# Kernel optimization log

Measured on AMD Instinct MI355X. Metric: run time of the kernel, lower is better.

## Reference

```python
import jax, jax.numpy as jnp
import numpy as np

N, F_IN, F_OUT = 8192, 512, 256
NEG_BIG = -9e15


def setup_inputs() -> dict:
    key = jax.random.key(0)
    k1, k2, k3, k4, k5 = jax.random.split(key, 5)
    h = jax.random.normal(k1, (N, F_IN), dtype=jnp.float32)
    adj = jax.random.randint(k2, (N, N), 0, 2, dtype=jnp.int32)
    W = jax.random.normal(k3, (F_IN, F_OUT), dtype=jnp.float32) / np.sqrt(F_IN)
    bW = jnp.zeros((F_OUT,), dtype=jnp.float32)
    a1 = jax.random.normal(k4, (F_OUT,), dtype=jnp.float32) / np.sqrt(2 * F_OUT)
    a2 = jax.random.normal(k5, (F_OUT,), dtype=jnp.float32) / np.sqrt(2 * F_OUT)
    ba = jnp.zeros((), dtype=jnp.float32)
    return {"h": h, "adj": adj, "W": W, "bW": bW, "a1": a1, "a2": a2, "ba": ba}


def reference(h, adj, W, bW, a1, a2, ba):
    # Wh: [N, F_OUT]
    Wh = h @ W + bW
    # a([Wh_i ; Wh_j]) + b == (Wh_i . a1) + (Wh_j . a2) + b  (rank-1 decomposition,
    # avoids the O(N^2 * 2F) repeat/cat tensor the torch code materializes)
    f1 = Wh @ a1  # [N]
    f2 = Wh @ a2  # [N]
    e = jax.nn.leaky_relu(f1[:, None] + f2[None, :] + ba, negative_slope=0.2)
    e = jnp.where(adj > 0, e, NEG_BIG)
    attention = jax.nn.softmax(e, axis=1)  # dropout = identity (eval mode)
    return attention @ Wh
```

## Files before the change

kernel.cpp:

```cpp
#include <hip/hip_runtime.h>

typedef __bf16 bf16;
typedef __attribute__((ext_vector_type(4))) float f32x4;
typedef __attribute__((ext_vector_type(8))) __bf16 bf16x8;
typedef __attribute__((ext_vector_type(4))) __bf16 bf16x4;
typedef __attribute__((ext_vector_type(4))) int i32x4;

#define NN 8192
#define FI 512
#define FO 256
#define NSPLIT 4
#define JCHUNK (NN / NSPLIT)

__global__ __launch_bounds__(256) void kw_split(const float* __restrict__ W,
                                                bf16* __restrict__ wth,
                                                bf16* __restrict__ wtl) {
  const int idx = blockIdx.x * 256 + threadIdx.x;
  const int k = idx >> 8, n = idx & 255;
  float x = W[idx];
  bf16 hi = (bf16)x;
  wth[(size_t)n * FI + k] = hi;
  wtl[(size_t)n * FI + k] = (bf16)(x - (float)hi);
}

__global__ __launch_bounds__(256, 2) void k1_gemm(
    const float* __restrict__ h, const bf16* __restrict__ wth,
    const bf16* __restrict__ wtl, const float* __restrict__ bW,
    const float* __restrict__ a1, const float* __restrict__ a2,
    bf16* __restrict__ whb, float* __restrict__ f1, float* __restrict__ f2) {
  __shared__ bf16 stg[128 * 32];
  const int t = threadIdx.x;
  const int lane = t & 63, w = t >> 6;
  const int m16 = lane & 15, q = lane >> 4;
  const int wr = w & 1, wn = w >> 1;
  const int rb = blockIdx.x, bj = blockIdx.y;
  const int row = rb * 32 + wr * 16 + m16;
  const int nb = bj * 128 + wn * 64;

  const f32x4 z4 = {0.f, 0.f, 0.f, 0.f};
  f32x4 acc[4];
#pragma unroll
  for (int nn = 0; nn < 4; ++nn) acc[nn] = z4;

  const float* hrow = h + (size_t)row * FI + q * 8;
  const bf16* wthp = wth + (size_t)(nb + m16) * FI + q * 8;
  const bf16* wtlp = wtl + (size_t)(nb + m16) * FI + q * 8;

  f32x4 nh0 = *(const f32x4*)(hrow);
  f32x4 nh1 = *(const f32x4*)(hrow + 4);

  const int KT = FI / 32;
  for (int kt = 0; kt < KT; ++kt) {
    bf16x8 bh[4], bl[4];
#pragma unroll
    for (int nn = 0; nn < 4; ++nn) {
      const size_t woff = (size_t)(nn * 16) * FI + kt * 32;
      bh[nn] = *(const bf16x8*)(wthp + woff);
      bl[nn] = *(const bf16x8*)(wtlp + woff);
    }
    const f32x4 h0 = nh0, h1 = nh1;
    const int ktn = (kt + 1 < KT) ? kt + 1 : kt;
    nh0 = *(const f32x4*)(hrow + ktn * 32);
    nh1 = *(const f32x4*)(hrow + ktn * 32 + 4);
    bf16x8 hh, hl;
#pragma unroll
    for (int x = 0; x < 4; ++x) {
      float v = h0[x];
      bf16 hi = (bf16)v;
      hh[x] = hi;
      hl[x] = (bf16)(v - (float)hi);
      float v2 = h1[x];
      bf16 hi2 = (bf16)v2;
      hh[4 + x] = hi2;
      hl[4 + x] = (bf16)(v2 - (float)hi2);
    }
#pragma unroll
    for (int nn = 0; nn < 4; ++nn) {
      acc[nn] = __builtin_amdgcn_mfma_f32_16x16x32_bf16(hh, bh[nn], acc[nn], 0, 0, 0);
      acc[nn] = __builtin_amdgcn_mfma_f32_16x16x32_bf16(hl, bh[nn], acc[nn], 0, 0, 0);
      acc[nn] = __builtin_amdgcn_mfma_f32_16x16x32_bf16(hh, bl[nn], acc[nn], 0, 0, 0);
    }
  }
  float f1p[4] = {}, f2p[4] = {};
  const int il = wr * 16 + q * 4;
#pragma unroll
  for (int nn = 0; nn < 4; ++nn) {
    const int n = nb + nn * 16 + m16;
    const int nl = wn * 64 + nn * 16 + m16;
    const float bw = bW[n], av1 = a1[n], av2 = a2[n];
    bf16x4 st;
#pragma unroll
    for (int reg = 0; reg < 4; ++reg) {
      float wh = acc[nn][reg] + bw;
      st[reg] = (bf16)wh;
      f1p[reg] += wh * av1;
      f2p[reg] += wh * av2;
    }
    *(bf16x4*)&stg[nl * 32 + il] = st;
  }
#pragma unroll
  for (int m = 1; m < 16; m <<= 1) {
#pragma unroll
    for (int reg = 0; reg < 4; ++reg) {
      f1p[reg] += __shfl_xor(f1p[reg], m);
      f2p[reg] += __shfl_xor(f2p[reg], m);
    }
  }
  if (m16 == 0) {
#pragma unroll
    for (int reg = 0; reg < 4; ++reg) {
      const int i = rb * 32 + wr * 16 + q * 4 + reg;
      atomicAdd(&f1[i], f1p[reg]);
      atomicAdd(&f2[i], f2p[reg]);
    }
  }
  __syncthreads();
  bf16x8* dst = (bf16x8*)(whb + (size_t)rb * (FO * 32) + (size_t)bj * (128 * 32));
  const bf16x8* srcv = (const bf16x8*)stg;
#pragma unroll
  for (int u = 0; u < 2; ++u) dst[t * 2 + u] = srcv[t * 2 + u];
}

__global__ __launch_bounds__(256, 4) void k4_attn(
    const int* __restrict__ adj, const bf16* __restrict__ whb,
    const float* __restrict__ f1, const float* __restrict__ f2,
    const float* __restrict__ ba_p,
    float* __restrict__ acc_part, float* __restrict__ l_part) {
  const int t = threadIdx.x;
  const int lane = t & 63, w = t >> 6;
  const int m16 = lane & 15, q = lane >> 4;
  const int wr = w & 1, wn = w >> 1;
  const int rb = blockIdx.x, s = blockIdx.y;
  const int i0 = rb * 32;
  const int row = i0 + wr * 16 + m16;

  const float ba = *ba_p;
  const float ci = f1[row] + ba;
  const float arg0 = ci + 8.0f;
  const float sh = fmaxf(arg0, 0.2f * arg0);

  const f32x4 z4 = {0.f, 0.f, 0.f, 0.f};
  f32x4 acc[8];
#pragma unroll
  for (int nn = 0; nn < 8; ++nn) acc[nn] = z4;
  float lreg = 0.f;

  const int sbase = s * JCHUNK;
  const int* arow = adj + (size_t)row * NN + sbase + q * 8;
  const float* frow = f2 + sbase + q * 8;
  const bf16* bptr = whb + (size_t)(sbase >> 5) * (FO * 32) +
                     (size_t)(wn * 128 + m16) * 32 + q * 8;

  i32x4 na0 = *(const i32x4*)(arow);
  i32x4 na1 = *(const i32x4*)(arow + 4);
  f32x4 nf0 = *(const f32x4*)(frow);
  f32x4 nf1 = *(const f32x4*)(frow + 4);

  const int KT = JCHUNK / 32;
  for (int kt = 0; kt < KT; ++kt) {
    bf16x8 cb[8];
    const bf16* bk = bptr + (size_t)kt * (FO * 32);
#pragma unroll
    for (int nn = 0; nn < 8; ++nn)
      cb[nn] = *(const bf16x8*)(bk + nn * (16 * 32));
    const i32x4 ca0 = na0;
    const i32x4 ca1 = na1;
    const f32x4 cf0 = nf0;
    const f32x4 cf1 = nf1;
    const int ktn = (kt + 1 < KT) ? kt + 1 : kt;
    na0 = *(const i32x4*)(arow + ktn * 32);
    na1 = *(const i32x4*)(arow + ktn * 32 + 4);
    nf0 = *(const f32x4*)(frow + ktn * 32);
    nf1 = *(const f32x4*)(frow + ktn * 32 + 4);
    float pv[8];
#pragma unroll
    for (int x = 0; x < 4; ++x) {
      float arg = ci + cf0[x];
      float e = fmaxf(arg, 0.2f * arg);
      pv[x] = (ca0[x] > 0) ? __expf(e - sh) : 0.f;
      float arg2 = ci + cf1[x];
      float e2 = fmaxf(arg2, 0.2f * arg2);
      pv[4 + x] = (ca1[x] > 0) ? __expf(e2 - sh) : 0.f;
    }
    bf16x8 af;
#pragma unroll
    for (int x = 0; x < 8; ++x) {
      lreg += pv[x];
      af[x] = (bf16)pv[x];
    }
#pragma unroll
    for (int nn = 0; nn < 8; ++nn)
      acc[nn] = __builtin_amdgcn_mfma_f32_16x16x32_bf16(af, cb[nn], acc[nn], 0, 0, 0);
  }
  lreg += __shfl_xor(lreg, 16);
  lreg += __shfl_xor(lreg, 32);
  if (q == 0 && wn == 0) l_part[(size_t)s * NN + row] = lreg;
  float* ap = acc_part + (size_t)s * ((size_t)NN * FO);
  const int r0 = i0 + wr * 16 + q * 4;
#pragma unroll
  for (int nn = 0; nn < 8; ++nn) {
    const int n = wn * 128 + nn * 16 + m16;
#pragma unroll
    for (int reg = 0; reg < 4; ++reg) {
      ap[(size_t)(r0 + reg) * FO + n] = acc[nn][reg];
    }
  }
}

__global__ __launch_bounds__(256) void k5_reduce(
    const float* __restrict__ accp, const float* __restrict__ lp,
    float* __restrict__ out) {
  const int idx = blockIdx.x * 256 + threadIdx.x;
  const int i = idx >> 6, n4 = (idx & 63) * 4;
  f32x4 sum = {0.f, 0.f, 0.f, 0.f};
  float l = 0.f;
#pragma unroll
  for (int s = 0; s < NSPLIT; ++s) {
    sum += *(const f32x4*)&accp[(size_t)s * ((size_t)NN * FO) + (size_t)i * FO + n4];
    l += lp[s * NN + i];
  }
  const float rl = 1.0f / l;
  f32x4 o = sum * rl;
  *(f32x4*)&out[(size_t)i * FO + n4] = o;
}

extern "C" void kernel_launch(void* const* d_in, const int* in_sizes, int n_in,
                              void* d_out, int out_size, void* d_ws, size_t ws_size,
                              hipStream_t stream) {
  const float* h   = (const float*)d_in[0];
  const int*   adj = (const int*)d_in[1];
  const float* W   = (const float*)d_in[2];
  const float* bW  = (const float*)d_in[3];
  const float* a1  = (const float*)d_in[4];
  const float* a2  = (const float*)d_in[5];
  const float* ba  = (const float*)d_in[6];
  float* out = (float*)d_out;

  char* ws = (char*)d_ws;
  bf16* whb   = (bf16*)ws;
  float* f1   = (float*)(ws + 4u * 1024 * 1024);
  float* f2   = (float*)(ws + 4u * 1024 * 1024 + 32 * 1024);
  float* accp = (float*)(ws + 4u * 1024 * 1024 + 64 * 1024);
  float* lp   = accp + (size_t)NSPLIT * NN * FO;
  bf16* wth   = (bf16*)((char*)lp + (size_t)NSPLIT * NN * 4);
  bf16* wtl   = wth + (size_t)FO * FI;

  hipMemsetAsync(f1, 0, 64 * 1024, stream);

  kw_split<<<FI * FO / 256, 256, 0, stream>>>(W, wth, wtl);
  k1_gemm<<<dim3(NN / 32, 2), 256, 0, stream>>>(h, wth, wtl, bW, a1, a2, whb, f1, f2);
  k4_attn<<<dim3(NN / 32, NSPLIT), 256, 0, stream>>>(adj, whb, f1, f2, ba, accp, lp);
  k5_reduce<<<(NN * FO / 4) / 256, 256, 0, stream>>>(accp, lp, out);
}
```

Measured before the change: 559.0 us.

## Split attention into score-materialization pass and full-K bf16 GEMM, drop split-K reduce

The fused attention kernel with a 4-way split-K and a separate reduce is replaced by two kernels. The first computes masked exp scores from adj and stores them as a bf16 P matrix in MFMA fragment layout, accumulating row sums atomically. The second runs a full-K GEMM of P against Wh, double-buffering its register loads, and writes normalized output directly. This removes the fp32 partial-accumulator writes and the reduce kernel, and gives the GEMM a cleaner load stream. The cost is a 128MB bf16 P write and re-read in exchange for the fp32 partials.

```diff
diff --git a/kernel.cpp b/kernel.cpp
--- a/kernel.cpp
+++ b/kernel.cpp
@@ -9,8 +9,8 @@
 #define NN 8192
 #define FI 512
 #define FO 256
-#define NSPLIT 4
-#define JCHUNK (NN / NSPLIT)
+
+#define MFMA16 __builtin_amdgcn_mfma_f32_16x16x32_bf16
 
 __global__ __launch_bounds__(256) void kw_split(const float* __restrict__ W,
                                                 bf16* __restrict__ wth,
@@ -76,9 +76,9 @@
     }
 #pragma unroll
     for (int nn = 0; nn < 4; ++nn) {
-      acc[nn] = __builtin_amdgcn_mfma_f32_16x16x32_bf16(hh, bh[nn], acc[nn], 0, 0, 0);
-      acc[nn] = __builtin_amdgcn_mfma_f32_16x16x32_bf16(hl, bh[nn], acc[nn], 0, 0, 0);
-      acc[nn] = __builtin_amdgcn_mfma_f32_16x16x32_bf16(hh, bl[nn], acc[nn], 0, 0, 0);
+      acc[nn] = MFMA16(hh, bh[nn], acc[nn], 0, 0, 0);
+      acc[nn] = MFMA16(hl, bh[nn], acc[nn], 0, 0, 0);
+      acc[nn] = MFMA16(hh, bl[nn], acc[nn], 0, 0, 0);
     }
   }
   float f1p[4] = {}, f2p[4] = {};
@@ -121,107 +121,125 @@
   for (int u = 0; u < 2; ++u) dst[t * 2 + u] = srcv[t * 2 + u];
 }
 
-__global__ __launch_bounds__(256, 4) void k4_attn(
-    const int* __restrict__ adj, const bf16* __restrict__ whb,
-    const float* __restrict__ f1, const float* __restrict__ f2,
-    const float* __restrict__ ba_p,
-    float* __restrict__ acc_part, float* __restrict__ l_part) {
+__global__ __launch_bounds__(256) void k4a_scores(
+    const int* __restrict__ adj, const float* __restrict__ f1,
+    const float* __restrict__ f2, const float* __restrict__ ba_p,
+    bf16* __restrict__ P, float* __restrict__ l) {
+  const int t = threadIdx.x;
+  const int lane = t & 63, w = t >> 6;
+  const int m16 = lane & 15, q = lane >> 4;
+  const int gw = blockIdx.x * 4 + w;
+  const int ib = gw >> 4;
+  const int js = gw & 15;
+  const int row = ib * 16 + m16;
+  const int j0 = js * 512;
+
+  const float ba = *ba_p;
+  const float ci = f1[row] + ba;
+  const float arg0 = ci + 8.0f;
+  const float sh = fmaxf(arg0, 0.2f * arg0);
+
+  const int* arow = adj + (size_t)row * NN + j0 + q * 8;
+  const float* frow = f2 + j0 + q * 8;
+  bf16* ptile = P + (size_t)(ib * 256 + js * 16) * 512 + lane * 8;
+
+  float lreg = 0.f;
+#pragma unroll 4
+  for (int jt = 0; jt < 16; ++jt) {
+    i32x4 a0 = *(const i32x4*)(arow + jt * 32);
+    i32x4 a1 = *(const i32x4*)(arow + jt * 32 + 4);
+    f32x4 g0 = *(const f32x4*)(frow + jt * 32);
+    f32x4 g1 = *(const f32x4*)(frow + jt * 32 + 4);
+    float pv[8];
+#pragma unroll
+    for (int x = 0; x < 4; ++x) {
+      float arg = ci + g0[x];
+      float e = fmaxf(arg, 0.2f * arg);
+      pv[x] = (a0[x] > 0) ? __expf(e - sh) : 0.f;
+      float arg2 = ci + g1[x];
+      float e2 = fmaxf(arg2, 0.2f * arg2);
+      pv[4 + x] = (a1[x] > 0) ? __expf(e2 - sh) : 0.f;
+    }
+    bf16x8 pb;
+#pragma unroll
+    for (int x = 0; x < 8; ++x) {
+      lreg += pv[x];
+      pb[x] = (bf16)pv[x];
+    }
+    *(bf16x8*)(ptile + (size_t)jt * 512) = pb;
+  }
+  lreg += __shfl_xor(lreg, 16);
+  lreg += __shfl_xor(lreg, 32);
+  if (q == 0) atomicAdd(&l[row], lreg);
+}
+
+__global__ __launch_bounds__(512, 2) void k4b_gemm(
+    const bf16* __restrict__ P, const bf16* __restrict__ whb,
+    const float* __restrict__ l, float* __restrict__ out) {
   const int t = threadIdx.x;
   const int lane = t & 63, w = t >> 6;
   const int m16 = lane & 15, q = lane >> 4;
   const int wr = w & 1, wn = w >> 1;
-  const int rb = blockIdx.x, s = blockIdx.y;
+  const int rb = blockIdx.x;
   const int i0 = rb * 32;
-  const int row = i0 + wr * 16 + m16;
-
-  const float ba = *ba_p;
-  const float ci = f1[row] + ba;
-  const float arg0 = ci + 8.0f;
-  const float sh = fmaxf(arg0, 0.2f * arg0);
+  const int itile = rb * 2 + wr;
+
+  const bf16* aptr = P + (size_t)itile * 256 * 512 + lane * 8;
+  const bf16* bptr = whb + (size_t)(wn * 64 + m16) * 32 + q * 8;
+  const size_t BSTRIDE = (size_t)FO * 32;
 
   const f32x4 z4 = {0.f, 0.f, 0.f, 0.f};
-  f32x4 acc[8];
-#pragma unroll
-  for (int nn = 0; nn < 8; ++nn) acc[nn] = z4;
-  float lreg = 0.f;
-
-  const int sbase = s * JCHUNK;
-  const int* arow = adj + (size_t)row * NN + sbase + q * 8;
-  const float* frow = f2 + sbase + q * 8;
-  const bf16* bptr = whb + (size_t)(sbase >> 5) * (FO * 32) +
-                     (size_t)(wn * 128 + m16) * 32 + q * 8;
-
-  i32x4 na0 = *(const i32x4*)(arow);
-  i32x4 na1 = *(const i32x4*)(arow + 4);
-  f32x4 nf0 = *(const f32x4*)(frow);
-  f32x4 nf1 = *(const f32x4*)(frow + 4);
-
-  const int KT = JCHUNK / 32;
-  for (int kt = 0; kt < KT; ++kt) {
-    bf16x8 cb[8];
-    const bf16* bk = bptr + (size_t)kt * (FO * 32);
-#pragma unroll
-    for (int nn = 0; nn < 8; ++nn)
-      cb[nn] = *(const bf16x8*)(bk + nn * (16 * 32));
-    const i32x4 ca0 = na0;
-    const i32x4 ca1 = na1;
-    const f32x4 cf0 = nf0;
-    const f32x4 cf1 = nf1;
-    const int ktn = (kt + 1 < KT) ? kt + 1 : kt;
-    na0 = *(const i32x4*)(arow + ktn * 32);
-    na1 = *(const i32x4*)(arow + ktn * 32 + 4);
-    nf0 = *(const f32x4*)(frow + ktn * 32);
-    nf1 = *(const f32x4*)(frow + ktn * 32 + 4);
-    float pv[8];
-#pragma unroll
-    for (int x = 0; x < 4; ++x) {
-      float arg = ci + cf0[x];
-      float e = fmaxf(arg, 0.2f * arg);
-      pv[x] = (ca0[x] > 0) ? __expf(e - sh) : 0.f;
-      float arg2 = ci + cf1[x];
-      float e2 = fmaxf(arg2, 0.2f * arg2);
-      pv[4 + x] = (ca1[x] > 0) ? __expf(e2 - sh) : 0.f;
-    }
-    bf16x8 af;
-#pragma unroll
-    for (int x = 0; x < 8; ++x) {
-      lreg += pv[x];
-      af[x] = (bf16)pv[x];
-    }
-#pragma unroll
-    for (int nn = 0; nn < 8; ++nn)
-      acc[nn] = __builtin_amdgcn_mfma_f32_16x16x32_bf16(af, cb[nn], acc[nn], 0, 0, 0);
-  }
-  lreg += __shfl_xor(lreg, 16);
-  lreg += __shfl_xor(lreg, 32);
-  if (q == 0 && wn == 0) l_part[(size_t)s * NN + row] = lreg;
-  float* ap = acc_part + (size_t)s * ((size_t)NN * FO);
+  f32x4 acc0 = z4, acc1 = z4, acc2 = z4, acc3 = z4;
+
+  bf16x8 aA = *(const bf16x8*)(aptr);
+  bf16x8 bA0 = *(const bf16x8*)(bptr);
+  bf16x8 bA1 = *(const bf16x8*)(bptr + 512);
+  bf16x8 bA2 = *(const bf16x8*)(bptr + 1024);
+  bf16x8 bA3 = *(const bf16x8*)(bptr + 1536);
+  bf16x8 aB, bB0, bB1, bB2, bB3;
+
+  const int KB = NN / 32;
+  for (int jb = 0; jb < KB; jb += 2) {
+    {
+      const int jn = jb + 1;
+      aB = *(const bf16x8*)(aptr + (size_t)jn * 512);
+      const bf16* bk = bptr + (size_t)jn * BSTRIDE;
+      bB0 = *(const bf16x8*)(bk);
+      bB1 = *(const bf16x8*)(bk + 512);
+      bB2 = *(const bf16x8*)(bk + 1024);
+      bB3 = *(const bf16x8*)(bk + 1536);
+      acc0 = MFMA16(aA, bA0, acc0, 0, 0, 0);
+      acc1 = MFMA16(aA, bA1, acc1, 0, 0, 0);
+      acc2 = MFMA16(aA, bA2, acc2, 0, 0, 0);
+      acc3 = MFMA16(aA, bA3, acc3, 0, 0, 0);
+    }
+    {
+      const int jn = (jb + 2 < KB) ? jb + 2 : 0;
+      aA = *(const bf16x8*)(aptr + (size_t)jn * 512);
+      const bf16* bk = bptr + (size_t)jn * BSTRIDE;
+      bA0 = *(const bf16x8*)(bk);
+      bA1 = *(const bf16x8*)(bk + 512);
+      bA2 = *(const bf16x8*)(bk + 1024);
+      bA3 = *(const bf16x8*)(bk + 1536);
+      acc0 = MFMA16(aB, bB0, acc0, 0, 0, 0);
+      acc1 = MFMA16(aB, bB1, acc1, 0, 0, 0);
+      acc2 = MFMA16(aB, bB2, acc2, 0, 0, 0);
+      acc3 = MFMA16(aB, bB3, acc3, 0, 0, 0);
+    }
+  }
   const int r0 = i0 + wr * 16 + q * 4;
-#pragma unroll
-  for (int nn = 0; nn < 8; ++nn) {
-    const int n = wn * 128 + nn * 16 + m16;
-#pragma unroll
-    for (int reg = 0; reg < 4; ++reg) {
-      ap[(size_t)(r0 + reg) * FO + n] = acc[nn][reg];
-    }
-  }
-}
-
-__global__ __launch_bounds__(256) void k5_reduce(
-    const float* __restrict__ accp, const float* __restrict__ lp,
-    float* __restrict__ out) {
-  const int idx = blockIdx.x * 256 + threadIdx.x;
-  const int i = idx >> 6, n4 = (idx & 63) * 4;
-  f32x4 sum = {0.f, 0.f, 0.f, 0.f};
-  float l = 0.f;
-#pragma unroll
-  for (int s = 0; s < NSPLIT; ++s) {
-    sum += *(const f32x4*)&accp[(size_t)s * ((size_t)NN * FO) + (size_t)i * FO + n4];
-    l += lp[s * NN + i];
-  }
-  const float rl = 1.0f / l;
-  f32x4 o = sum * rl;
-  *(f32x4*)&out[(size_t)i * FO + n4] = o;
+  float rl[4];
+#pragma unroll
+  for (int reg = 0; reg < 4; ++reg) rl[reg] = 1.0f / l[r0 + reg];
+  f32x4 accs[4] = {acc0, acc1, acc2, acc3};
+#pragma unroll
+  for (int nn = 0; nn < 4; ++nn) {
+    const int n = wn * 64 + nn * 16 + m16;
+#pragma unroll
+    for (int reg = 0; reg < 4; ++reg) {
+      out[(size_t)(r0 + reg) * FO + n] = accs[nn][reg] * rl[reg];
+    }
+  }
 }
 
 extern "C" void kernel_launch(void* const* d_in, const int* in_sizes, int n_in,
@@ -237,18 +255,18 @@
   float* out = (float*)d_out;
 
   char* ws = (char*)d_ws;
-  bf16* whb   = (bf16*)ws;
-  float* f1   = (float*)(ws + 4u * 1024 * 1024);
-  float* f2   = (float*)(ws + 4u * 1024 * 1024 + 32 * 1024);
-  float* accp = (float*)(ws + 4u * 1024 * 1024 + 64 * 1024);
-  float* lp   = accp + (size_t)NSPLIT * NN * FO;
-  bf16* wth   = (bf16*)((char*)lp + (size_t)NSPLIT * NN * 4);
-  bf16* wtl   = wth + (size_t)FO * FI;
-
-  hipMemsetAsync(f1, 0, 64 * 1024, stream);
+  bf16* whb = (bf16*)ws;
+  float* f1 = (float*)(ws + 4u * 1024 * 1024);
+  float* f2 = (float*)(ws + 4u * 1024 * 1024 + 32 * 1024);
+  float* l  = (float*)(ws + 4u * 1024 * 1024 + 64 * 1024);
+  bf16* wth = (bf16*)(ws + 4u * 1024 * 1024 + 96 * 1024);
+  bf16* wtl = wth + (size_t)FO * FI;
+  bf16* P   = (bf16*)(ws + 8u * 1024 * 1024);
+
+  hipMemsetAsync(f1, 0, 96 * 1024, stream);
 
   kw_split<<<FI * FO / 256, 256, 0, stream>>>(W, wth, wtl);
   k1_gemm<<<dim3(NN / 32, 2), 256, 0, stream>>>(h, wth, wtl, bW, a1, a2, whb, f1, f2);
-  k4_attn<<<dim3(NN / 32, NSPLIT), 256, 0, stream>>>(adj, whb, f1, f2, ba, accp, lp);
-  k5_reduce<<<(NN * FO / 4) / 256, 256, 0, stream>>>(accp, lp, out);
-}
+  k4a_scores<<<NN / 4, 256, 0, stream>>>(adj, f1, f2, ba, P, l);
+  k4b_gemm<<<NN / 32, 512, 0, stream>>>(P, whb, l, out);
+}
```

Result: slower. 775.6 us (+38.8%).
